# Kernel tuning notes

Measured on AMD Instinct MI355X. Metric: run time of the kernel, lower is better.

The kernel has to match this reference:

```python
import jax, jax.numpy as jnp
import numpy as np

B, S, G, E = 2048, 32768, 4096, 1024  # batch, source_size, n_groups(target_size), embeddings_size


def setup_inputs() -> dict:
    key = jax.random.key(0)
    k_x, k_w, k_we, k_perm = jax.random.split(key, 4)
    x = jax.random.normal(k_x, (B, S), dtype=jnp.float32)
    W = jax.random.normal(k_w, (E, G), dtype=jnp.float32) * 0.02  # Linear(target_size -> embed, no bias)
    # per-element weights for 'w_sum' groups (concatenated Linear(group_size,1) weights)
    w_elem = jax.random.normal(k_we, (S,), dtype=jnp.float32) * 0.1
    perm = jax.random.permutation(k_perm, S).astype(jnp.int32)
    # ragged group boundaries: n_groups groups, each size >= 1, summing to S
    rng = np.random.default_rng(0)
    cuts = np.sort(rng.choice(np.arange(1, S), G - 1, replace=False))
    sizes = np.diff(np.concatenate([[0], cuts, [S]]))
    segment_ids = jnp.asarray(np.repeat(np.arange(G), sizes), dtype=jnp.int32)
    # aggregation type per group: 0='sum', 1='or', 2='w_sum'
    agg_type = jnp.asarray(rng.integers(0, 3, G), dtype=jnp.int32)
    return {"x": x, "W": W, "w_elem": w_elem, "perm": perm,
            "segment_ids": segment_ids, "agg_type": agg_type}


def reference(x, W, w_elem, perm, segment_ids, agg_type):
    # gather via groups_permute
    xp = x[:, perm]  # [B, S]
    # fused ragged per-group reductions, segment axis first: [S, B] -> [G, B]
    xt = xp.T
    seg_sum = jax.ops.segment_sum(xt, segment_ids, num_segments=G)              # jnp.sum per group
    seg_wsum = jax.ops.segment_sum(xt * w_elem[:, None], segment_ids, num_segments=G)  # Linear(g,1) per group
    seg_nnz = jax.ops.segment_sum((xt != 0).astype(x.dtype), segment_ids, num_segments=G)
    seg_or = (seg_nnz > 0).astype(x.dtype)                                       # jnp.any per group (bool -> float on hstack)
    a = agg_type[:, None]
    y = jnp.where(a == 0, seg_sum, jnp.where(a == 1, seg_or, seg_wsum)).T        # [B, G]
    # relu + Linear(target_size -> embeddings_size, no bias)
    return jnp.einsum('bg,eg->be', jax.nn.relu(y), W)
```

## Files before the change

kernel.cpp:

```cpp
#include <hip/hip_runtime.h>
#include <hip/hip_bf16.h>

#define B_DIM 2048
#define S_DIM 32768
#define G_DIM 4096
#define E_DIM 1024
#define KSPLIT 4
#define KCHUNK (G_DIM / KSPLIT)

typedef __bf16 bf16x8 __attribute__((ext_vector_type(8)));
typedef float f32x4 __attribute__((ext_vector_type(4)));

__device__ __forceinline__ unsigned short f2bf(float f) {
  unsigned int u = __builtin_bit_cast(unsigned int, f);
  u += 0x7FFFu + ((u >> 16) & 1u);
  return (unsigned short)(u >> 16);
}

__device__ __forceinline__ float bfl(unsigned u) {
  return __builtin_bit_cast(float, u << 16);
}
__device__ __forceinline__ float bfh(unsigned u) {
  return __builtin_bit_cast(float, u & 0xFFFF0000u);
}

__device__ __forceinline__ void async16(void* lds, const void* g) {
  __builtin_amdgcn_global_load_lds(
      (const __attribute__((address_space(1))) unsigned int*)g,
      (__attribute__((address_space(3))) unsigned int*)lds, 16, 0, 0);
}

__global__ __launch_bounds__(256) void setup_meta(
    const float* __restrict__ w_elem, const int* __restrict__ perm,
    const int* __restrict__ segid, const int* __restrict__ agg,
    unsigned* __restrict__ meta1) {
  int s = blockIdx.x * 256 + threadIdx.x;
  if (s >= S_DIM) return;
  int g = segid[s];
  int a = agg[g];
  float cm = (a == 0) ? 1.0f : (a == 2 ? w_elem[s] : 0.0f);
  meta1[s] = (unsigned)perm[s] | (a == 1 ? 0x8000u : 0u) |
             ((unsigned)f2bf(cm) << 16);
}

__global__ __launch_bounds__(256) void setup_runs(
    const int* __restrict__ segid, unsigned* __restrict__ metaH,
    unsigned short* __restrict__ metaG) {
  int t = blockIdx.x * 256 + threadIdx.x;
  if (t >= S_DIM / 32) return;
  int s0 = t * 32;
  int prev = (s0 == 0) ? -1 : segid[s0 - 1];
  unsigned m = 0;
#pragma unroll
  for (int c = 0; c < 8; ++c) {
    int4 gw = *reinterpret_cast<const int4*>(segid + s0 + c * 4);
    if (gw.x != prev) m |= 1u << (c * 4 + 0);
    if (gw.y != gw.x) m |= 1u << (c * 4 + 1);
    if (gw.z != gw.y) m |= 1u << (c * 4 + 2);
    if (gw.w != gw.z) m |= 1u << (c * 4 + 3);
    prev = gw.w;
  }
  metaH[t] = m;
  metaG[t] = (unsigned short)segid[s0];
}

__global__ __launch_bounds__(256) void conv_w(const float* __restrict__ W,
                                              unsigned short* __restrict__ Wb) {
  size_t i = ((size_t)blockIdx.x * 256 + threadIdx.x) * 4;
  float4 v = *reinterpret_cast<const float4*>(W + i);
  ushort4 o;
  o.x = f2bf(v.x);
  o.y = f2bf(v.y);
  o.z = f2bf(v.z);
  o.w = f2bf(v.w);
  *reinterpret_cast<ushort4*>(Wb + i) = o;
}

__global__ __launch_bounds__(1024, 8) void seg_reduce(
    const float* __restrict__ x, const unsigned* __restrict__ meta1,
    const unsigned* __restrict__ metaH, const unsigned short* __restrict__ metaG,
    const int* __restrict__ agg, unsigned short* __restrict__ y) {
  __shared__ __align__(16) unsigned short xrow[S_DIM];
  __shared__ float acc[G_DIM];
  float* scr = reinterpret_cast<float*>(xrow);
  const int t = threadIdx.x;
  const int b = blockIdx.x;

#pragma unroll
  for (int i = 0; i < G_DIM / 1024; ++i) acc[t + i * 1024] = 0.0f;

  const unsigned mrun = metaH[t];
  const unsigned nextH = (t < 1023) ? metaH[t + 1] : 1u;
  const bool fp = (mrun & 1u) != 0;
  int g = metaG[t];

  const float4* xg = reinterpret_cast<const float4*>(x + (size_t)b * S_DIM);
#pragma unroll
  for (int i = 0; i < S_DIM / 4 / 1024; ++i) {
    float4 v = xg[i * 1024 + t];
    unsigned short h0 = __builtin_bit_cast(unsigned short, (__bf16)v.x);
    unsigned short h1 = __builtin_bit_cast(unsigned short, (__bf16)v.y);
    unsigned short h2 = __builtin_bit_cast(unsigned short, (__bf16)v.z);
    unsigned short h3 = __builtin_bit_cast(unsigned short, (__bf16)v.w);
    uint2 p;
    p.x = (unsigned)h0 | ((unsigned)h1 << 16);
    p.y = (unsigned)h2 | ((unsigned)h3 << 16);
    *reinterpret_cast<uint2*>(&xrow[(i * 1024 + t) * 4]) = p;
  }
  __syncthreads();

  const int s0 = t * 32;
  float sum = 0.0f, lead = 0.0f;
  int nf = 0;

  for (int h = 0; h < 2; ++h) {
    const int sb = s0 + h * 16;
    uint4 ma = *reinterpret_cast<const uint4*>(meta1 + sb);
    uint4 mb = *reinterpret_cast<const uint4*>(meta1 + sb + 4);
    uint4 mc = *reinterpret_cast<const uint4*>(meta1 + sb + 8);
    uint4 md = *reinterpret_cast<const uint4*>(meta1 + sb + 12);
    unsigned m[16] = {ma.x, ma.y, ma.z, ma.w, mb.x, mb.y, mb.z, mb.w,
                      mc.x, mc.y, mc.z, mc.w, md.x, md.y, md.z, md.w};
    unsigned short xu[16];
#pragma unroll
    for (int j = 0; j < 16; ++j) xu[j] = xrow[m[j] & 0x7FFF];
    const unsigned mh = mrun >> (h * 16);
#pragma unroll
    for (int j = 0; j < 16; ++j) {
      if (h + j > 0 && (mh & (1u << j))) {
        if (nf == 0 && !fp) {
          lead = sum;
        } else {
          acc[g] = sum;
        }
        ++nf;
        sum = 0.0f;
        ++g;
      }
      float xv = bfl((unsigned)xu[j]);
      float cm = bfh(m[j]);
      float v = (m[j] & 0x8000u) ? (xu[j] ? 1.0f : 0.0f) : xv * cm;
      sum += v;
    }
  }

  __syncthreads();

  scr[t] = fp ? 0.0f : (nf == 0 ? sum : lead);
  __syncthreads();

  if (mrun != 0) {
    float tot = sum;
    unsigned fh = nextH;
    int k = t + 1;
    while (k < 1024) {
      tot += scr[k];
      if (fh) break;
      ++k;
      fh = metaH[k];
    }
    acc[g] = tot;
  }
  __syncthreads();

#pragma unroll
  for (int i = 0; i < G_DIM / 1024; ++i) {
    int g2 = t + i * 1024;
    float v = acc[g2];
    if (agg[g2] == 1) v = (v > 0.0f) ? 1.0f : 0.0f;
    v = fmaxf(v, 0.0f);
    y[(size_t)b * G_DIM + g2] = f2bf(v);
  }
}

__global__ __launch_bounds__(256) void gemm_bt(
    const unsigned short* __restrict__ A,
    const unsigned short* __restrict__ Bw,
    unsigned short* __restrict__ part) {
  __shared__ __align__(16) unsigned short As[64 * 64];
  __shared__ __align__(16) unsigned short Bs[64 * 64];
  const int t = threadIdx.x;
  const int lane = t & 63;
  const int wid = t >> 6;
  const int wr = wid >> 1;
  const int wc = wid & 1;
  const int row0 = blockIdx.y * 64;
  const int col0 = blockIdx.x * 64;
  const int kc = blockIdx.z;

  const int r_ = t >> 3;
  const int s_ = t & 7;
  const int ksw = (s_ ^ (r_ & 7)) * 8;
  const unsigned short* Ag0 = A + (size_t)(row0 + r_) * G_DIM + ksw;
  const unsigned short* Ag1 = A + (size_t)(row0 + r_ + 32) * G_DIM + ksw;
  const unsigned short* Bg0 = Bw + (size_t)(col0 + r_) * G_DIM + ksw;
  const unsigned short* Bg1 = Bw + (size_t)(col0 + r_ + 32) * G_DIM + ksw;

  char* AsB = (char*)As;
  char* BsB = (char*)Bs;
  char* dA0 = AsB + wid * 1024;
  char* dA1 = AsB + 4096 + wid * 1024;
  char* dB0 = BsB + wid * 1024;
  char* dB1 = BsB + 4096 + wid * 1024;

  const int lm = lane & 15;
  const int lk = lane >> 4;

  f32x4 acc[2][2] = {};

  for (int kt = kc * KCHUNK; kt < (kc + 1) * KCHUNK; kt += 64) {
    async16(dA0, Ag0 + kt);
    async16(dA1, Ag1 + kt);
    async16(dB0, Bg0 + kt);
    async16(dB1, Bg1 + kt);
    __syncthreads();
#pragma unroll
    for (int kk = 0; kk < 2; ++kk) {
      bf16x8 af[2], bfr[2];
#pragma unroll
      for (int m = 0; m < 2; ++m) {
        int row = wr * 32 + m * 16 + lm;
        int slot = (kk * 4 + lk) ^ (row & 7);
        af[m] = *(const bf16x8*)(AsB + row * 128 + slot * 16);
      }
#pragma unroll
      for (int n = 0; n < 2; ++n) {
        int row = wc * 32 + n * 16 + lm;
        int slot = (kk * 4 + lk) ^ (row & 7);
        bfr[n] = *(const bf16x8*)(BsB + row * 128 + slot * 16);
      }
#pragma unroll
      for (int m = 0; m < 2; ++m)
#pragma unroll
        for (int n = 0; n < 2; ++n)
          acc[m][n] = __builtin_amdgcn_mfma_f32_16x16x32_bf16(af[m], bfr[n],
                                                              acc[m][n], 0, 0, 0);
    }
    __syncthreads();
  }

  unsigned short* P = part + (size_t)kc * B_DIM * E_DIM;
#pragma unroll
  for (int m = 0; m < 2; ++m) {
    int r = row0 + wr * 32 + m * 16 + lk * 4;
#pragma unroll
    for (int n = 0; n < 2; ++n) {
      int c = col0 + wc * 32 + n * 16 + lm;
#pragma unroll
      for (int q = 0; q < 4; ++q) {
        P[(size_t)(r + q) * E_DIM + c] = f2bf(acc[m][n][q]);
      }
    }
  }
}

__global__ __launch_bounds__(256) void reduce_part(
    const unsigned short* __restrict__ part, float* __restrict__ C) {
  const size_t i = ((size_t)blockIdx.x * 256 + threadIdx.x) * 8;
  const size_t n = (size_t)B_DIM * E_DIM;
  float e[8] = {};
#pragma unroll
  for (int p = 0; p < KSPLIT; ++p) {
    uint4 v = *reinterpret_cast<const uint4*>(part + p * n + i);
    unsigned w[4] = {v.x, v.y, v.z, v.w};
#pragma unroll
    for (int q = 0; q < 4; ++q) {
      e[2 * q] += bfl(w[q]);
      e[2 * q + 1] += bfh(w[q]);
    }
  }
  float4 o0 = {e[0], e[1], e[2], e[3]};
  float4 o1 = {e[4], e[5], e[6], e[7]};
  *reinterpret_cast<float4*>(C + i) = o0;
  *reinterpret_cast<float4*>(C + i + 4) = o1;
}

extern "C" void kernel_launch(void* const* d_in, const int* in_sizes, int n_in,
                              void* d_out, int out_size, void* d_ws, size_t ws_size,
                              hipStream_t stream) {
  const float* x = (const float*)d_in[0];
  const float* W = (const float*)d_in[1];
  const float* w_elem = (const float*)d_in[2];
  const int* perm = (const int*)d_in[3];
  const int* segid = (const int*)d_in[4];
  const int* agg = (const int*)d_in[5];
  float* out = (float*)d_out;

  char* ws = (char*)d_ws;
  unsigned short* y = (unsigned short*)ws;
  unsigned short* Wb =
      (unsigned short*)(ws + (size_t)B_DIM * G_DIM * 2);
  unsigned short* part =
      (unsigned short*)(ws + (size_t)B_DIM * G_DIM * 2 +
                        (size_t)E_DIM * G_DIM * 2);
  unsigned* meta1 =
      (unsigned*)((char*)part + (size_t)KSPLIT * B_DIM * E_DIM * 2);
  unsigned* metaH = (unsigned*)((char*)meta1 + (size_t)S_DIM * 4);
  unsigned short* metaG = (unsigned short*)((char*)metaH + (S_DIM / 32) * 4);

  hipLaunchKernelGGL(setup_meta, dim3(S_DIM / 256), dim3(256), 0, stream,
                     w_elem, perm, segid, agg, meta1);
  hipLaunchKernelGGL(setup_runs, dim3((S_DIM / 32) / 256), dim3(256), 0,
                     stream, segid, metaH, metaG);
  hipLaunchKernelGGL(conv_w, dim3((E_DIM * G_DIM / 4) / 256), dim3(256), 0,
                     stream, W, Wb);
  hipLaunchKernelGGL(seg_reduce, dim3(B_DIM), dim3(1024), 0, stream, x, meta1,
                     metaH, metaG, agg, y);
  hipLaunchKernelGGL(gemm_bt, dim3(E_DIM / 64, B_DIM / 64, KSPLIT), dim3(256),
                     0, stream, y, Wb, part);
  hipLaunchKernelGGL(reduce_part,
                     dim3(((size_t)B_DIM * E_DIM / 8) / 256), dim3(256), 0,
                     stream, part, out);
}
```

Baseline: 126.0 us.

## Process multiple batch rows per seg_reduce block with register prefetch of next row

Each seg_reduce block now handles 8 batch rows, keeping per-thread metadata (meta1, agg) in registers so it is loaded once and reused across rows. The next row of x is prefetched into registers while the current row is gathered and reduced, then written into LDS after the row finishes. This amortizes metadata loads and hides global load latency, but the grid shrinks to 256 blocks of 1024 threads and register pressure grows, which may lower occupancy and parallelism.

```diff
diff --git a/kernel.cpp b/kernel.cpp
--- a/kernel.cpp
+++ b/kernel.cpp
@@ -7,6 +7,7 @@
 #define E_DIM 1024
 #define KSPLIT 4
 #define KCHUNK (G_DIM / KSPLIT)
+#define ROWS 8
 
 typedef __bf16 bf16x8 __attribute__((ext_vector_type(8)));
 typedef float f32x4 __attribute__((ext_vector_type(4)));
@@ -28,6 +29,15 @@
   __builtin_amdgcn_global_load_lds(
       (const __attribute__((address_space(1))) unsigned int*)g,
       (__attribute__((address_space(3))) unsigned int*)lds, 16, 0, 0);
+}
+
+__device__ __forceinline__ uint2 pack4bf(float4 v) {
+  uint2 r;
+  r.x = (unsigned)__builtin_bit_cast(unsigned short, (__bf16)v.x) |
+        ((unsigned)__builtin_bit_cast(unsigned short, (__bf16)v.y) << 16);
+  r.y = (unsigned)__builtin_bit_cast(unsigned short, (__bf16)v.z) |
+        ((unsigned)__builtin_bit_cast(unsigned short, (__bf16)v.w) << 16);
+  return r;
 }
 
 __global__ __launch_bounds__(256) void setup_meta(
@@ -76,7 +86,7 @@
   *reinterpret_cast<ushort4*>(Wb + i) = o;
 }
 
-__global__ __launch_bounds__(1024, 8) void seg_reduce(
+__global__ __launch_bounds__(1024) void seg_reduce(
     const float* __restrict__ x, const unsigned* __restrict__ meta1,
     const unsigned* __restrict__ metaH, const unsigned short* __restrict__ metaG,
     const int* __restrict__ agg, unsigned short* __restrict__ y) {
@@ -84,92 +94,121 @@
   __shared__ float acc[G_DIM];
   float* scr = reinterpret_cast<float*>(xrow);
   const int t = threadIdx.x;
-  const int b = blockIdx.x;
-
-#pragma unroll
-  for (int i = 0; i < G_DIM / 1024; ++i) acc[t + i * 1024] = 0.0f;
+  const int b0 = blockIdx.x * ROWS;
 
   const unsigned mrun = metaH[t];
   const unsigned nextH = (t < 1023) ? metaH[t + 1] : 1u;
   const bool fp = (mrun & 1u) != 0;
-  int g = metaG[t];
-
-  const float4* xg = reinterpret_cast<const float4*>(x + (size_t)b * S_DIM);
-#pragma unroll
-  for (int i = 0; i < S_DIM / 4 / 1024; ++i) {
-    float4 v = xg[i * 1024 + t];
-    unsigned short h0 = __builtin_bit_cast(unsigned short, (__bf16)v.x);
-    unsigned short h1 = __builtin_bit_cast(unsigned short, (__bf16)v.y);
-    unsigned short h2 = __builtin_bit_cast(unsigned short, (__bf16)v.z);
-    unsigned short h3 = __builtin_bit_cast(unsigned short, (__bf16)v.w);
-    uint2 p;
-    p.x = (unsigned)h0 | ((unsigned)h1 << 16);
-    p.y = (unsigned)h2 | ((unsigned)h3 << 16);
-    *reinterpret_cast<uint2*>(&xrow[(i * 1024 + t) * 4]) = p;
+  const int g0 = metaG[t];
+  const int a0 = agg[t];
+  const int a1 = agg[t + 1024];
+  const int a2 = agg[t + 2048];
+  const int a3 = agg[t + 3072];
+
+  uint4 mr[8];
+#pragma unroll
+  for (int q = 0; q < 8; ++q)
+    mr[q] = *reinterpret_cast<const uint4*>(meta1 + t * 32 + q * 4);
+
+  {
+    const float4* xg = reinterpret_cast<const float4*>(x + (size_t)b0 * S_DIM);
+#pragma unroll
+    for (int i = 0; i < 8; ++i) {
+      uint2 p = pack4bf(xg[i * 1024 + t]);
+      *reinterpret_cast<uint2*>(&xrow[(i * 1024 + t) * 4]) = p;
+    }
   }
   __syncthreads();
 
-  const int s0 = t * 32;
-  float sum = 0.0f, lead = 0.0f;
-  int nf = 0;
-
-  for (int h = 0; h < 2; ++h) {
-    const int sb = s0 + h * 16;
-    uint4 ma = *reinterpret_cast<const uint4*>(meta1 + sb);
-    uint4 mb = *reinterpret_cast<const uint4*>(meta1 + sb + 4);
-    uint4 mc = *reinterpret_cast<const uint4*>(meta1 + sb + 8);
-    uint4 md = *reinterpret_cast<const uint4*>(meta1 + sb + 12);
-    unsigned m[16] = {ma.x, ma.y, ma.z, ma.w, mb.x, mb.y, mb.z, mb.w,
-                      mc.x, mc.y, mc.z, mc.w, md.x, md.y, md.z, md.w};
-    unsigned short xu[16];
-#pragma unroll
-    for (int j = 0; j < 16; ++j) xu[j] = xrow[m[j] & 0x7FFF];
-    const unsigned mh = mrun >> (h * 16);
-#pragma unroll
-    for (int j = 0; j < 16; ++j) {
-      if (h + j > 0 && (mh & (1u << j))) {
-        if (nf == 0 && !fp) {
-          lead = sum;
-        } else {
-          acc[g] = sum;
+  for (int r = 0; r < ROWS; ++r) {
+    const bool pf = (r < ROWS - 1);
+    const float4* xgn =
+        reinterpret_cast<const float4*>(x + (size_t)(b0 + r + 1) * S_DIM);
+    float4 nxa[4], nxb[4];
+    if (pf) {
+#pragma unroll
+      for (int i = 0; i < 4; ++i) nxa[i] = xgn[i * 1024 + t];
+    }
+
+    int g = g0;
+    float sum = 0.0f, lead = 0.0f;
+    int nf = 0;
+#pragma unroll
+    for (int q = 0; q < 8; ++q) {
+      if (q == 4 && pf) {
+#pragma unroll
+        for (int i = 0; i < 4; ++i) nxb[i] = xgn[(4 + i) * 1024 + t];
+      }
+      unsigned m4[4] = {mr[q].x, mr[q].y, mr[q].z, mr[q].w};
+      unsigned short xu[4];
+#pragma unroll
+      for (int j = 0; j < 4; ++j) xu[j] = xrow[m4[j] & 0x7FFF];
+      const unsigned mh = mrun >> (q * 4);
+#pragma unroll
+      for (int j = 0; j < 4; ++j) {
+        if (q * 4 + j > 0 && (mh & (1u << j))) {
+          if (nf == 0 && !fp) {
+            lead = sum;
+          } else {
+            acc[g] = sum;
+          }
+          ++nf;
+          sum = 0.0f;
+          ++g;
         }
-        ++nf;
-        sum = 0.0f;
-        ++g;
-      }
-      float xv = bfl((unsigned)xu[j]);
-      float cm = bfh(m[j]);
-      float v = (m[j] & 0x8000u) ? (xu[j] ? 1.0f : 0.0f) : xv * cm;
-      sum += v;
-    }
-  }
-
-  __syncthreads();
-
-  scr[t] = fp ? 0.0f : (nf == 0 ? sum : lead);
-  __syncthreads();
-
-  if (mrun != 0) {
-    float tot = sum;
-    unsigned fh = nextH;
-    int k = t + 1;
-    while (k < 1024) {
-      tot += scr[k];
-      if (fh) break;
-      ++k;
-      fh = metaH[k];
-    }
-    acc[g] = tot;
-  }
-  __syncthreads();
-
-#pragma unroll
-  for (int i = 0; i < G_DIM / 1024; ++i) {
-    int g2 = t + i * 1024;
-    float v = acc[g2];
-    if (agg[g2] == 1) v = (v > 0.0f) ? 1.0f : 0.0f;
-    v = fmaxf(v, 0.0f);
-    y[(size_t)b * G_DIM + g2] = f2bf(v);
+        float xv = bfl((unsigned)xu[j]);
+        float cm = bfh(m4[j]);
+        float v = (m4[j] & 0x8000u) ? (xu[j] ? 1.0f : 0.0f) : xv * cm;
+        sum += v;
+      }
+    }
+    __syncthreads();
+
+    scr[t] = fp ? 0.0f : (nf == 0 ? sum : lead);
+    __syncthreads();
+
+    if (mrun != 0) {
+      float tot = sum;
+      unsigned fh = nextH;
+      int k = t + 1;
+      while (k < 1024) {
+        tot += scr[k];
+        if (fh) break;
+        ++k;
+        fh = metaH[k];
+      }
+      acc[g] = tot;
+    }
+    __syncthreads();
+
+    {
+      const size_t yb = (size_t)(b0 + r) * G_DIM;
+      float v0 = acc[t];
+      float v1 = acc[t + 1024];
+      float v2 = acc[t + 2048];
+      float v3 = acc[t + 3072];
+      if (a0 == 1) v0 = (v0 > 0.0f) ? 1.0f : 0.0f;
+      if (a1 == 1) v1 = (v1 > 0.0f) ? 1.0f : 0.0f;
+      if (a2 == 1) v2 = (v2 > 0.0f) ? 1.0f : 0.0f;
+      if (a3 == 1) v3 = (v3 > 0.0f) ? 1.0f : 0.0f;
+      y[yb + t] = f2bf(fmaxf(v0, 0.0f));
+      y[yb + t + 1024] = f2bf(fmaxf(v1, 0.0f));
+      y[yb + t + 2048] = f2bf(fmaxf(v2, 0.0f));
+      y[yb + t + 3072] = f2bf(fmaxf(v3, 0.0f));
+    }
+    if (pf) {
+#pragma unroll
+      for (int i = 0; i < 4; ++i) {
+        uint2 p = pack4bf(nxa[i]);
+        *reinterpret_cast<uint2*>(&xrow[(i * 1024 + t) * 4]) = p;
+      }
+#pragma unroll
+      for (int i = 0; i < 4; ++i) {
+        uint2 p = pack4bf(nxb[i]);
+        *reinterpret_cast<uint2*>(&xrow[((4 + i) * 1024 + t) * 4]) = p;
+      }
+    }
+    __syncthreads();
   }
 }
 
@@ -304,8 +343,8 @@
                      stream, segid, metaH, metaG);
   hipLaunchKernelGGL(conv_w, dim3((E_DIM * G_DIM / 4) / 256), dim3(256), 0,
                      stream, W, Wb);
-  hipLaunchKernelGGL(seg_reduce, dim3(B_DIM), dim3(1024), 0, stream, x, meta1,
-                     metaH, metaG, agg, y);
+  hipLaunchKernelGGL(seg_reduce, dim3(B_DIM / ROWS), dim3(1024), 0, stream, x,
+                     meta1, metaH, metaG, agg, y);
   hipLaunchKernelGGL(gemm_bt, dim3(E_DIM / 64, B_DIM / 64, KSPLIT), dim3(256),
                      0, stream, y, Wb, part);
   hipLaunchKernelGGL(reduce_part,
```

Measured after the change: 186.7 us. 1.48x slower.
